# Kernel optimization log

Hardware: AMD Instinct MI355X
Metric: run time of the kernel (lower is better)

## Reference

```python
import jax, jax.numpy as jnp
import numpy as np

B, D, H = 65536, 64, 512  # batch, input_dim (even), hidden_dim; num_layers=4 -> 4 Linears


def setup_inputs() -> dict:
    key = jax.random.key(0)
    ks = jax.random.split(key, 10)
    s_in = 1.0 / np.sqrt(D)
    s_h = 1.0 / np.sqrt(H)
    return {
        "t": jnp.zeros((1,), jnp.float32),
        "x": jax.random.normal(ks[0], (B, D), jnp.float32),
        "W0": jax.random.uniform(ks[1], (D, H), jnp.float32, -s_in, s_in),
        "b0": jax.random.uniform(ks[2], (H,), jnp.float32, -s_in, s_in),
        "W1": jax.random.uniform(ks[3], (H, H), jnp.float32, -s_h, s_h),
        "b1": jax.random.uniform(ks[4], (H,), jnp.float32, -s_h, s_h),
        "W2": jax.random.uniform(ks[5], (H, H), jnp.float32, -s_h, s_h),
        "b2": jax.random.uniform(ks[6], (H,), jnp.float32, -s_h, s_h),
        "W3": jax.random.uniform(ks[7], (H, 1), jnp.float32, -s_h, s_h),
        "b3": jax.random.uniform(ks[8], (1,), jnp.float32, -s_h, s_h),
    }


def reference(t, x, W0, b0, W1, b1, W2, b2, W3, b3):
    # Hamiltonian MLP: Linear->Tanh x3, final Linear to scalar energy per sample.
    def hamiltonian_sum(xx):
        h = jnp.tanh(xx @ W0 + b0)
        h = jnp.tanh(h @ W1 + b1)
        h = jnp.tanh(h @ W2 + b2)
        return jnp.sum(h @ W3 + b3)

    gradH = jax.grad(hamiltonian_sum)(x)  # [B, D]
    n = D // 2
    # gradH @ J.T with symplectic J == concat(gradH_p, -gradH_q)
    return jnp.concatenate([gradH[:, n:], -gradH[:, :n]], axis=1)
```

## Files before the change

kernel.cpp:

```cpp
#include <hip/hip_runtime.h>
#include <hip/hip_bf16.h>

typedef unsigned short u16;
typedef short s16x8 __attribute__((ext_vector_type(8)));
typedef float f32x4 __attribute__((ext_vector_type(4)));

#define MFMA_BF16(a, b, c) __builtin_amdgcn_mfma_f32_16x16x32_bf16((a), (b), (c), 0, 0, 0)

static constexpr int D_IN   = 64;
static constexpr int H_DIM  = 512;
static constexpr int M_TILE = 64;
static constexpr int AST    = 520;
static constexpr int XST    = 72;

__device__ __forceinline__ u16 f2bf(float f) {
  unsigned u = __builtin_bit_cast(unsigned, f);
  u += 0x7fffu + ((u >> 16) & 1u);
  return (u16)(u >> 16);
}
__device__ __forceinline__ float bfb2f(unsigned bits16) {
  return __builtin_bit_cast(float, bits16 << 16);
}
__device__ __forceinline__ float fast_tanh(float x) {
  float e = __expf(2.0f * x);
  return 1.0f - 2.0f * __builtin_amdgcn_rcpf(e + 1.0f);
}

__global__ __launch_bounds__(256) void prep_weights(const float* __restrict__ W0,
                                                    const float* __restrict__ W1,
                                                    const float* __restrict__ W2,
                                                    u16* __restrict__ ws) {
  u16* p0f = ws;
  u16* p0b = p0f + D_IN * H_DIM;
  u16* p1f = p0b + D_IN * H_DIM;
  u16* p1b = p1f + H_DIM * H_DIM;
  u16* p2f = p1b + H_DIM * H_DIM;
  u16* p2b = p2f + H_DIM * H_DIM;

  __shared__ __align__(16) u16 tile[64 * 72];

  int b = blockIdx.x;
  const float* src;
  u16 *dstf, *dstb;
  int rb, cb;
  bool isW0;
  if (b < 64) {
    src = W1; dstf = p1f; dstb = p1b; rb = b >> 3; cb = b & 7; isW0 = false;
  } else if (b < 128) {
    src = W2; dstf = p2f; dstb = p2b; rb = (b - 64) >> 3; cb = (b - 64) & 7; isW0 = false;
  } else {
    src = W0; dstf = p0f; dstb = p0b; rb = 0; cb = b - 128; isW0 = true;
  }

  const int tid = threadIdx.x;

  {
    int r = tid >> 2, cc = (tid & 3) * 16;
    const float4* s4 = (const float4*)(src + (size_t)(rb * 64 + r) * 512 + cb * 64 + cc);
    unsigned pk[8];
    #pragma unroll
    for (int v = 0; v < 4; ++v) {
      float4 f = s4[v];
      pk[v * 2]     = (unsigned)f2bf(f.x) | ((unsigned)f2bf(f.y) << 16);
      pk[v * 2 + 1] = (unsigned)f2bf(f.z) | ((unsigned)f2bf(f.w) << 16);
    }
    uint4* d = (uint4*)(tile + r * 72 + cc);
    d[0] = make_uint4(pk[0], pk[1], pk[2], pk[3]);
    d[1] = make_uint4(pk[4], pk[5], pk[6], pk[7]);
  }
  __syncthreads();

  const int c   = tid >> 6;
  const int kcl = (tid >> 5) & 1;
  const int ls  = (tid * 2) & 63;
  const int q   = ls >> 4;
  const int ln  = ls & 15;

  {
    __align__(16) u16 o[16];
    #pragma unroll
    for (int half = 0; half < 2; ++half)
      #pragma unroll
      for (int j = 0; j < 8; ++j)
        o[half * 8 + j] = tile[(kcl * 32 + q * 8 + j) * 72 + c * 16 + ln + half];
    int ntg   = 4 * cb + c;
    int kc    = 2 * rb + kcl;
    int chunk = isW0 ? (ntg * 2 + kc) : (ntg * 16 + kc);
    u16* dp = dstf + ((size_t)chunk * 64 + ls) * 8;
    *(uint4*)dp       = *(const uint4*)o;
    *(uint4*)(dp + 8) = *(const uint4*)(o + 8);
  }

  {
    const u16* rp = tile + (c * 16 + ln) * 72 + kcl * 32 + q * 8;
    s16x8 r0 = *(const s16x8*)rp;
    s16x8 r1 = *(const s16x8*)(rp + 72);
    int ntg = 4 * rb + c;
    int kc  = 2 * cb + kcl;
    u16* dp = dstb + ((size_t)(ntg * 16 + kc) * 64 + ls) * 8;
    *(s16x8*)dp       = r0;
    *(s16x8*)(dp + 8) = r1;
  }
}

#define LOAD_B4(BP, KC, BR)                                                     \
  {                                                                             \
    const u16* _sr = (BP) + ((size_t)wave << 15) + ((KC) << 9) + lane * 8;      \
    _Pragma("unroll")                                                           \
    for (int s = 0; s < 4; ++s)                                                 \
      (BR)[s] = *(const s16x8*)(_sr + (s << 13));                               \
  }

#define GEMM512_REG(BP, RB)                                                     \
  {                                                                             \
    _Pragma("unroll") for (int mt = 0; mt < 4; ++mt)                            \
      _Pragma("unroll") for (int nt = 0; nt < 4; ++nt)                          \
        acc[mt][nt] = (f32x4){0.f, 0.f, 0.f, 0.f};                              \
    for (int kc2 = 0; kc2 < 8; ++kc2) {                                         \
      const int e = kc2 * 2;                                                    \
      {                                                                         \
        s16x8 a[4];                                                             \
        _Pragma("unroll")                                                       \
        for (int mt = 0; mt < 4; ++mt)                                          \
          a[mt] = *(const s16x8*)((RB) + (mt * 16 + ln) * AST + e * 32 + q * 8);\
        _Pragma("unroll")                                                       \
        for (int nt = 0; nt < 4; ++nt)                                          \
          _Pragma("unroll")                                                     \
          for (int mt = 0; mt < 4; ++mt)                                        \
            acc[mt][nt] = MFMA_BF16(a[mt], bregA[nt], acc[mt][nt]);             \
        if (kc2 < 7) LOAD_B4(BP, e + 2, bregA);                                 \
      }                                                                         \
      const int o = e + 1;                                                      \
      {                                                                         \
        s16x8 a[4];                                                             \
        _Pragma("unroll")                                                       \
        for (int mt = 0; mt < 4; ++mt)                                          \
          a[mt] = *(const s16x8*)((RB) + (mt * 16 + ln) * AST + o * 32 + q * 8);\
        _Pragma("unroll")                                                       \
        for (int nt = 0; nt < 4; ++nt)                                          \
          _Pragma("unroll")                                                     \
          for (int mt = 0; mt < 4; ++mt)                                        \
            acc[mt][nt] = MFMA_BF16(a[mt], bregB[nt], acc[mt][nt]);             \
        if (kc2 < 7) LOAD_B4(BP, o + 2, bregB);                                 \
      }                                                                         \
    }                                                                           \
  }

__global__ __launch_bounds__(512, 2) void hnn_fused(
    const float* __restrict__ x,
    const float* __restrict__ bias0,
    const float* __restrict__ bias1,
    const float* __restrict__ bias2,
    const float* __restrict__ W3,
    const u16* __restrict__ ws,
    float* __restrict__ out)
{
  const u16* p0f = ws;
  const u16* p0b = p0f + D_IN * H_DIM;
  const u16* p1f = p0b + D_IN * H_DIM;
  const u16* p1b = p1f + H_DIM * H_DIM;
  const u16* p2f = p1b + H_DIM * H_DIM;
  const u16* p2b = p2f + H_DIM * H_DIM;

  __shared__ __align__(16) u16 xs[M_TILE * XST];
  __shared__ __align__(16) u16 bufA[M_TILE * AST];
  __shared__ __align__(16) u16 bufB[M_TILE * AST];

  const int tid  = threadIdx.x;
  const int wave = tid >> 6;
  const int lane = tid & 63;
  const int ln   = lane & 15;
  const int q    = lane >> 4;
  const int nwb  = wave * 64;
  const int row0 = blockIdx.x * M_TILE;

  {
    int r = tid >> 3, c = (tid & 7) * 8;
    const float4* src = (const float4*)(x + (size_t)(row0 + r) * D_IN + c);
    float4 f0 = src[0];
    float4 f1 = src[1];
    u16* dst = xs + r * XST + c;
    dst[0] = f2bf(f0.x); dst[1] = f2bf(f0.y); dst[2] = f2bf(f0.z); dst[3] = f2bf(f0.w);
    dst[4] = f2bf(f1.x); dst[5] = f2bf(f1.y); dst[6] = f2bf(f1.z); dst[7] = f2bf(f1.w);
  }
  __syncthreads();

  f32x4 acc[4][4];
  s16x8 bregA[4], bregB[4];
  unsigned h0p[4][4][2];
  unsigned h1p[4][4][2];
  float bias[4];

  #pragma unroll
  for (int nt = 0; nt < 4; ++nt) bias[nt] = bias0[nwb + nt * 16 + ln];
  #pragma unroll
  for (int mt = 0; mt < 4; ++mt)
    #pragma unroll
    for (int nt = 0; nt < 4; ++nt) acc[mt][nt] = (f32x4){0.f, 0.f, 0.f, 0.f};
  {
    const u16* bpw0 = p0f + (wave << 12) + lane * 8;
    #pragma unroll
    for (int kc = 0; kc < 2; ++kc) {
      s16x8 a[4];
      #pragma unroll
      for (int mt = 0; mt < 4; ++mt)
        a[mt] = *(const s16x8*)(xs + (mt * 16 + ln) * XST + kc * 32 + q * 8);
      #pragma unroll
      for (int nt = 0; nt < 4; ++nt) {
        s16x8 b = *(const s16x8*)(bpw0 + (nt << 10) + (kc << 9));
        #pragma unroll
        for (int mt = 0; mt < 4; ++mt)
          acc[mt][nt] = MFMA_BF16(a[mt], b, acc[mt][nt]);
      }
    }
  }
  LOAD_B4(p1f, 0, bregA);
  LOAD_B4(p1f, 1, bregB);
  #pragma unroll
  for (int mt = 0; mt < 4; ++mt)
    #pragma unroll
    for (int nt = 0; nt < 4; ++nt) {
      int col = nwb + nt * 16 + ln;
      u16 u[4];
      #pragma unroll
      for (int r = 0; r < 4; ++r) {
        float th = fast_tanh(acc[mt][nt][r] + bias[nt]);
        u[r] = f2bf(th);
        bufA[(mt * 16 + q * 4 + r) * AST + col] = u[r];
      }
      h0p[mt][nt][0] = (unsigned)u[0] | ((unsigned)u[1] << 16);
      h0p[mt][nt][1] = (unsigned)u[2] | ((unsigned)u[3] << 16);
    }
  __syncthreads();

  #pragma unroll
  for (int nt = 0; nt < 4; ++nt) bias[nt] = bias1[nwb + nt * 16 + ln];
  GEMM512_REG(p1f, bufA);
  LOAD_B4(p2f, 0, bregA);
  LOAD_B4(p2f, 1, bregB);
  #pragma unroll
  for (int mt = 0; mt < 4; ++mt)
    #pragma unroll
    for (int nt = 0; nt < 4; ++nt) {
      int col = nwb + nt * 16 + ln;
      u16 u[4];
      #pragma unroll
      for (int r = 0; r < 4; ++r) {
        float th = fast_tanh(acc[mt][nt][r] + bias[nt]);
        u[r] = f2bf(th);
        bufB[(mt * 16 + q * 4 + r) * AST + col] = u[r];
      }
      h1p[mt][nt][0] = (unsigned)u[0] | ((unsigned)u[1] << 16);
      h1p[mt][nt][1] = (unsigned)u[2] | ((unsigned)u[3] << 16);
    }
  __syncthreads();

  #pragma unroll
  for (int nt = 0; nt < 4; ++nt) bias[nt] = bias2[nwb + nt * 16 + ln];
  float w3v[4];
  #pragma unroll
  for (int nt = 0; nt < 4; ++nt) w3v[nt] = W3[nwb + nt * 16 + ln];
  GEMM512_REG(p2f, bufB);
  LOAD_B4(p2b, 0, bregA);
  LOAD_B4(p2b, 1, bregB);
  #pragma unroll
  for (int mt = 0; mt < 4; ++mt)
    #pragma unroll
    for (int nt = 0; nt < 4; ++nt) {
      int col = nwb + nt * 16 + ln;
      #pragma unroll
      for (int r = 0; r < 4; ++r) {
        float th = fast_tanh(acc[mt][nt][r] + bias[nt]);
        float gz = w3v[nt] * (1.0f - th * th);
        bufA[(mt * 16 + q * 4 + r) * AST + col] = f2bf(gz);
      }
    }
  __syncthreads();

  GEMM512_REG(p2b, bufA);
  LOAD_B4(p1b, 0, bregA);
  LOAD_B4(p1b, 1, bregB);
  #pragma unroll
  for (int mt = 0; mt < 4; ++mt)
    #pragma unroll
    for (int nt = 0; nt < 4; ++nt) {
      int col = nwb + nt * 16 + ln;
      unsigned pa = h1p[mt][nt][0], pb = h1p[mt][nt][1];
      float hh[4] = { bfb2f(pa & 0xffffu), bfb2f(pa >> 16),
                      bfb2f(pb & 0xffffu), bfb2f(pb >> 16) };
      #pragma unroll
      for (int r = 0; r < 4; ++r) {
        float gz = acc[mt][nt][r] * (1.0f - hh[r] * hh[r]);
        bufB[(mt * 16 + q * 4 + r) * AST + col] = f2bf(gz);
      }
    }
  __syncthreads();

  GEMM512_REG(p1b, bufB);
  __syncthreads();
  #pragma unroll
  for (int mt = 0; mt < 4; ++mt)
    #pragma unroll
    for (int nt = 0; nt < 4; ++nt) {
      int col = nwb + nt * 16 + ln;
      unsigned pa = h0p[mt][nt][0], pb = h0p[mt][nt][1];
      float hh[4] = { bfb2f(pa & 0xffffu), bfb2f(pa >> 16),
                      bfb2f(pb & 0xffffu), bfb2f(pb >> 16) };
      #pragma unroll
      for (int r = 0; r < 4; ++r) {
        float gz = acc[mt][nt][r] * (1.0f - hh[r] * hh[r]);
        bufA[(mt * 16 + q * 4 + r) * AST + col] = f2bf(gz);
      }
    }
  __syncthreads();

  {
    f32x4 acc5[2];
    acc5[0] = (f32x4){0.f, 0.f, 0.f, 0.f};
    acc5[1] = (f32x4){0.f, 0.f, 0.f, 0.f};
    const int mt5 = wave & 3;
    const int nb5 = (wave >> 2) * 32;
    const u16* bp5 = p0b + ((wave >> 2) << 14) + lane * 8;
    #pragma unroll 2
    for (int kc = 0; kc < 16; ++kc) {
      s16x8 a = *(const s16x8*)(bufA + (mt5 * 16 + ln) * AST + kc * 32 + q * 8);
      #pragma unroll
      for (int nt = 0; nt < 2; ++nt) {
        s16x8 b = *(const s16x8*)(bp5 + (nt << 13) + (kc << 9));
        acc5[nt] = MFMA_BF16(a, b, acc5[nt]);
      }
    }
    #pragma unroll
    for (int nt = 0; nt < 2; ++nt) {
      int g = nb5 + nt * 16 + ln;
      int c = (g < 32) ? g + 32 : g - 32;
      float s = (g < 32) ? -1.0f : 1.0f;
      #pragma unroll
      for (int r = 0; r < 4; ++r) {
        int grow = row0 + mt5 * 16 + q * 4 + r;
        out[(size_t)grow * 64 + c] = s * acc5[nt][r];
      }
    }
  }
}

extern "C" void kernel_launch(void* const* d_in, const int* in_sizes, int n_in,
                              void* d_out, int out_size, void* d_ws, size_t ws_size,
                              hipStream_t stream) {
  const float* x  = (const float*)d_in[1];
  const float* W0 = (const float*)d_in[2];
  const float* b0 = (const float*)d_in[3];
  const float* W1 = (const float*)d_in[4];
  const float* b1 = (const float*)d_in[5];
  const float* W2 = (const float*)d_in[6];
  const float* b2 = (const float*)d_in[7];
  const float* W3 = (const float*)d_in[8];
  u16* ws = (u16*)d_ws;
  float* out = (float*)d_out;

  prep_weights<<<136, 256, 0, stream>>>(W0, W1, W2, ws);
  hnn_fused<<<65536 / M_TILE, 512, 0, stream>>>(x, b0, b1, b2, W3, ws, out);
}
```

Measured before the change: 223.9 us.

## Shrink row tile to 32 with 4 waves each covering 128 columns

Halves the block row tile to 32 and the block to 4 waves, with each wave now owning 128 hidden columns (8 N-subtiles) over 2 M-subtiles. This roughly halves LDS per block and changes the register tiling so each weight fragment loaded from global memory feeds fewer MFMAs (2 instead of 4), while doubling the number of blocks. A redundant barrier before the last backward epilogue is also removed. Register pressure rises (acc, breg and h arrays double per wave), which may limit occupancy, and per-row weight traffic from L2 doubles.

```diff
diff --git a/kernel.cpp b/kernel.cpp
--- a/kernel.cpp
+++ b/kernel.cpp
@@ -9,7 +9,7 @@
 
 static constexpr int D_IN   = 64;
 static constexpr int H_DIM  = 512;
-static constexpr int M_TILE = 64;
+static constexpr int M_TILE = 32;
 static constexpr int AST    = 520;
 static constexpr int XST    = 72;
 
@@ -103,50 +103,50 @@
   }
 }
 
-#define LOAD_B4(BP, KC, BR)                                                     \
+#define LOAD_B8(BP, KC, BR)                                                     \
   {                                                                             \
-    const u16* _sr = (BP) + ((size_t)wave << 15) + ((KC) << 9) + lane * 8;      \
+    const u16* _sr = (BP) + ((size_t)wave << 16) + ((KC) << 9) + lane * 8;      \
     _Pragma("unroll")                                                           \
-    for (int s = 0; s < 4; ++s)                                                 \
+    for (int s = 0; s < 8; ++s)                                                 \
       (BR)[s] = *(const s16x8*)(_sr + (s << 13));                               \
   }
 
 #define GEMM512_REG(BP, RB)                                                     \
   {                                                                             \
-    _Pragma("unroll") for (int mt = 0; mt < 4; ++mt)                            \
-      _Pragma("unroll") for (int nt = 0; nt < 4; ++nt)                          \
+    _Pragma("unroll") for (int mt = 0; mt < 2; ++mt)                            \
+      _Pragma("unroll") for (int nt = 0; nt < 8; ++nt)                          \
         acc[mt][nt] = (f32x4){0.f, 0.f, 0.f, 0.f};                              \
     for (int kc2 = 0; kc2 < 8; ++kc2) {                                         \
       const int e = kc2 * 2;                                                    \
       {                                                                         \
-        s16x8 a[4];                                                             \
+        s16x8 a[2];                                                             \
         _Pragma("unroll")                                                       \
-        for (int mt = 0; mt < 4; ++mt)                                          \
+        for (int mt = 0; mt < 2; ++mt)                                          \
           a[mt] = *(const s16x8*)((RB) + (mt * 16 + ln) * AST + e * 32 + q * 8);\
         _Pragma("unroll")                                                       \
-        for (int nt = 0; nt < 4; ++nt)                                          \
+        for (int nt = 0; nt < 8; ++nt)                                          \
           _Pragma("unroll")                                                     \
-          for (int mt = 0; mt < 4; ++mt)                                        \
+          for (int mt = 0; mt < 2; ++mt)                                        \
             acc[mt][nt] = MFMA_BF16(a[mt], bregA[nt], acc[mt][nt]);             \
-        if (kc2 < 7) LOAD_B4(BP, e + 2, bregA);                                 \
+        if (kc2 < 7) LOAD_B8(BP, e + 2, bregA);                                 \
       }                                                                         \
       const int o = e + 1;                                                      \
       {                                                                         \
-        s16x8 a[4];                                                             \
+        s16x8 a[2];                                                             \
         _Pragma("unroll")                                                       \
-        for (int mt = 0; mt < 4; ++mt)                                          \
+        for (int mt = 0; mt < 2; ++mt)                                          \
           a[mt] = *(const s16x8*)((RB) + (mt * 16 + ln) * AST + o * 32 + q * 8);\
         _Pragma("unroll")                                                       \
-        for (int nt = 0; nt < 4; ++nt)                                          \
+        for (int nt = 0; nt < 8; ++nt)                                          \
           _Pragma("unroll")                                                     \
-          for (int mt = 0; mt < 4; ++mt)                                        \
+          for (int mt = 0; mt < 2; ++mt)                                        \
             acc[mt][nt] = MFMA_BF16(a[mt], bregB[nt], acc[mt][nt]);             \
-        if (kc2 < 7) LOAD_B4(BP, o + 2, bregB);                                 \
+        if (kc2 < 7) LOAD_B8(BP, o + 2, bregB);                                 \
       }                                                                         \
     }                                                                           \
   }
 
-__global__ __launch_bounds__(512, 2) void hnn_fused(
+__global__ __launch_bounds__(256, 2) void hnn_fused(
     const float* __restrict__ x,
     const float* __restrict__ bias0,
     const float* __restrict__ bias1,
@@ -171,7 +171,7 @@
   const int lane = tid & 63;
   const int ln   = lane & 15;
   const int q    = lane >> 4;
-  const int nwb  = wave * 64;
+  const int nwb  = wave * 128;
   const int row0 = blockIdx.x * M_TILE;
 
   {
@@ -185,41 +185,41 @@
   }
   __syncthreads();
 
-  f32x4 acc[4][4];
-  s16x8 bregA[4], bregB[4];
-  unsigned h0p[4][4][2];
-  unsigned h1p[4][4][2];
-  float bias[4];
-
-  #pragma unroll
-  for (int nt = 0; nt < 4; ++nt) bias[nt] = bias0[nwb + nt * 16 + ln];
-  #pragma unroll
-  for (int mt = 0; mt < 4; ++mt)
-    #pragma unroll
-    for (int nt = 0; nt < 4; ++nt) acc[mt][nt] = (f32x4){0.f, 0.f, 0.f, 0.f};
-  {
-    const u16* bpw0 = p0f + (wave << 12) + lane * 8;
+  f32x4 acc[2][8];
+  s16x8 bregA[8], bregB[8];
+  unsigned h0p[2][8][2];
+  unsigned h1p[2][8][2];
+  float bias[8];
+
+  #pragma unroll
+  for (int nt = 0; nt < 8; ++nt) bias[nt] = bias0[nwb + nt * 16 + ln];
+  #pragma unroll
+  for (int mt = 0; mt < 2; ++mt)
+    #pragma unroll
+    for (int nt = 0; nt < 8; ++nt) acc[mt][nt] = (f32x4){0.f, 0.f, 0.f, 0.f};
+  {
+    const u16* bpw0 = p0f + ((size_t)wave << 13) + lane * 8;
     #pragma unroll
     for (int kc = 0; kc < 2; ++kc) {
-      s16x8 a[4];
-      #pragma unroll
-      for (int mt = 0; mt < 4; ++mt)
+      s16x8 a[2];
+      #pragma unroll
+      for (int mt = 0; mt < 2; ++mt)
         a[mt] = *(const s16x8*)(xs + (mt * 16 + ln) * XST + kc * 32 + q * 8);
       #pragma unroll
-      for (int nt = 0; nt < 4; ++nt) {
+      for (int nt = 0; nt < 8; ++nt) {
         s16x8 b = *(const s16x8*)(bpw0 + (nt << 10) + (kc << 9));
         #pragma unroll
-        for (int mt = 0; mt < 4; ++mt)
+        for (int mt = 0; mt < 2; ++mt)
           acc[mt][nt] = MFMA_BF16(a[mt], b, acc[mt][nt]);
       }
     }
   }
-  LOAD_B4(p1f, 0, bregA);
-  LOAD_B4(p1f, 1, bregB);
-  #pragma unroll
-  for (int mt = 0; mt < 4; ++mt)
-    #pragma unroll
-    for (int nt = 0; nt < 4; ++nt) {
+  LOAD_B8(p1f, 0, bregA);
+  LOAD_B8(p1f, 1, bregB);
+  #pragma unroll
+  for (int mt = 0; mt < 2; ++mt)
+    #pragma unroll
+    for (int nt = 0; nt < 8; ++nt) {
       int col = nwb + nt * 16 + ln;
       u16 u[4];
       #pragma unroll
@@ -234,14 +234,14 @@
   __syncthreads();
 
   #pragma unroll
-  for (int nt = 0; nt < 4; ++nt) bias[nt] = bias1[nwb + nt * 16 + ln];
+  for (int nt = 0; nt < 8; ++nt) bias[nt] = bias1[nwb + nt * 16 + ln];
   GEMM512_REG(p1f, bufA);
-  LOAD_B4(p2f, 0, bregA);
-  LOAD_B4(p2f, 1, bregB);
-  #pragma unroll
-  for (int mt = 0; mt < 4; ++mt)
-    #pragma unroll
-    for (int nt = 0; nt < 4; ++nt) {
+  LOAD_B8(p2f, 0, bregA);
+  LOAD_B8(p2f, 1, bregB);
+  #pragma unroll
+  for (int mt = 0; mt < 2; ++mt)
+    #pragma unroll
+    for (int nt = 0; nt < 8; ++nt) {
       int col = nwb + nt * 16 + ln;
       u16 u[4];
       #pragma unroll
@@ -256,17 +256,17 @@
   __syncthreads();
 
   #pragma unroll
-  for (int nt = 0; nt < 4; ++nt) bias[nt] = bias2[nwb + nt * 16 + ln];
-  float w3v[4];
-  #pragma unroll
-  for (int nt = 0; nt < 4; ++nt) w3v[nt] = W3[nwb + nt * 16 + ln];
+  for (int nt = 0; nt < 8; ++nt) bias[nt] = bias2[nwb + nt * 16 + ln];
+  float w3v[8];
+  #pragma unroll
+  for (int nt = 0; nt < 8; ++nt) w3v[nt] = W3[nwb + nt * 16 + ln];
   GEMM512_REG(p2f, bufB);
-  LOAD_B4(p2b, 0, bregA);
-  LOAD_B4(p2b, 1, bregB);
-  #pragma unroll
-  for (int mt = 0; mt < 4; ++mt)
-    #pragma unroll
-    for (int nt = 0; nt < 4; ++nt) {
+  LOAD_B8(p2b, 0, bregA);
+  LOAD_B8(p2b, 1, bregB);
+  #pragma unroll
+  for (int mt = 0; mt < 2; ++mt)
+    #pragma unroll
+    for (int nt = 0; nt < 8; ++nt) {
       int col = nwb + nt * 16 + ln;
       #pragma unroll
       for (int r = 0; r < 4; ++r) {
@@ -278,12 +278,12 @@
   __syncthreads();
 
   GEMM512_REG(p2b, bufA);
-  LOAD_B4(p1b, 0, bregA);
-  LOAD_B4(p1b, 1, bregB);
-  #pragma unroll
-  for (int mt = 0; mt < 4; ++mt)
-    #pragma unroll
-    for (int nt = 0; nt < 4; ++nt) {
+  LOAD_B8(p1b, 0, bregA);
+  LOAD_B8(p1b, 1, bregB);
+  #pragma unroll
+  for (int mt = 0; mt < 2; ++mt)
+    #pragma unroll
+    for (int nt = 0; nt < 8; ++nt) {
       int col = nwb + nt * 16 + ln;
       unsigned pa = h1p[mt][nt][0], pb = h1p[mt][nt][1];
       float hh[4] = { bfb2f(pa & 0xffffu), bfb2f(pa >> 16),
@@ -297,11 +297,10 @@
   __syncthreads();
 
   GEMM512_REG(p1b, bufB);
-  __syncthreads();
-  #pragma unroll
-  for (int mt = 0; mt < 4; ++mt)
-    #pragma unroll
-    for (int nt = 0; nt < 4; ++nt) {
+  #pragma unroll
+  for (int mt = 0; mt < 2; ++mt)
+    #pragma unroll
+    for (int nt = 0; nt < 8; ++nt) {
       int col = nwb + nt * 16 + ln;
       unsigned pa = h0p[mt][nt][0], pb = h0p[mt][nt][1];
       float hh[4] = { bfb2f(pa & 0xffffu), bfb2f(pa >> 16),
@@ -318,27 +317,27 @@
     f32x4 acc5[2];
     acc5[0] = (f32x4){0.f, 0.f, 0.f, 0.f};
     acc5[1] = (f32x4){0.f, 0.f, 0.f, 0.f};
-    const int mt5 = wave & 3;
-    const int nb5 = (wave >> 2) * 32;
-    const u16* bp5 = p0b + ((wave >> 2) << 14) + lane * 8;
+    const int mt5 = wave & 1;
+    const int np5 = (wave >> 1) * 2;
+    const u16* bp5 = p0b + ((size_t)np5 << 13) + lane * 8;
     #pragma unroll 2
     for (int kc = 0; kc < 16; ++kc) {
       s16x8 a = *(const s16x8*)(bufA + (mt5 * 16 + ln) * AST + kc * 32 + q * 8);
       #pragma unroll
-      for (int nt = 0; nt < 2; ++nt) {
-        s16x8 b = *(const s16x8*)(bp5 + (nt << 13) + (kc << 9));
-        acc5[nt] = MFMA_BF16(a, b, acc5[nt]);
-      }
-    }
-    #pragma unroll
-    for (int nt = 0; nt < 2; ++nt) {
-      int g = nb5 + nt * 16 + ln;
+      for (int i = 0; i < 2; ++i) {
+        s16x8 b = *(const s16x8*)(bp5 + (i << 13) + (kc << 9));
+        acc5[i] = MFMA_BF16(a, b, acc5[i]);
+      }
+    }
+    #pragma unroll
+    for (int i = 0; i < 2; ++i) {
+      int g = (np5 + i) * 16 + ln;
       int c = (g < 32) ? g + 32 : g - 32;
       float s = (g < 32) ? -1.0f : 1.0f;
       #pragma unroll
       for (int r = 0; r < 4; ++r) {
         int grow = row0 + mt5 * 16 + q * 4 + r;
-        out[(size_t)grow * 64 + c] = s * acc5[nt][r];
+        out[(size_t)grow * 64 + c] = s * acc5[i][r];
       }
     }
   }
@@ -359,5 +358,5 @@
   float* out = (float*)d_out;
 
   prep_weights<<<136, 256, 0, stream>>>(W0, W1, W2, ws);
-  hnn_fused<<<65536 / M_TILE, 512, 0, stream>>>(x, b0, b1, b2, W3, ws, out);
-}
+  hnn_fused<<<65536 / M_TILE, 256, 0, stream>>>(x, b0, b1, b2, W3, ws, out);
+}
```

Result: slower. 575.1 us (+156.9%).

## Halve row tile to 32 and raise occupancy to four blocks per CU

Applied to the files above, without the earlier changes.

Cuts the per-block row tile from 64 to 32, which halves the accumulator and saved-activation register arrays and lets launch bounds request four blocks per CU. The x load, the final input-gradient GEMM's wave-to-tile mapping and the epilogue are rewritten for the smaller tile, and one redundant barrier is dropped. The aim is more waves in flight to hide the latency of weight loads from global memory. In exchange each B-fragment loaded from global now feeds only half as many MFMAs, doubling weight traffic per row. Shared memory per block is also still fixed by AST and may limit how many blocks actually co-reside.

```diff
diff --git a/kernel.cpp b/kernel.cpp
--- a/kernel.cpp
+++ b/kernel.cpp
@@ -9,7 +9,7 @@
 
 static constexpr int D_IN   = 64;
 static constexpr int H_DIM  = 512;
-static constexpr int M_TILE = 64;
+static constexpr int M_TILE = 32;
 static constexpr int AST    = 520;
 static constexpr int XST    = 72;
 
@@ -113,40 +113,40 @@
 
 #define GEMM512_REG(BP, RB)                                                     \
   {                                                                             \
-    _Pragma("unroll") for (int mt = 0; mt < 4; ++mt)                            \
+    _Pragma("unroll") for (int mt = 0; mt < 2; ++mt)                            \
       _Pragma("unroll") for (int nt = 0; nt < 4; ++nt)                          \
         acc[mt][nt] = (f32x4){0.f, 0.f, 0.f, 0.f};                              \
     for (int kc2 = 0; kc2 < 8; ++kc2) {                                         \
       const int e = kc2 * 2;                                                    \
       {                                                                         \
-        s16x8 a[4];                                                             \
+        s16x8 a[2];                                                             \
         _Pragma("unroll")                                                       \
-        for (int mt = 0; mt < 4; ++mt)                                          \
+        for (int mt = 0; mt < 2; ++mt)                                          \
           a[mt] = *(const s16x8*)((RB) + (mt * 16 + ln) * AST + e * 32 + q * 8);\
         _Pragma("unroll")                                                       \
         for (int nt = 0; nt < 4; ++nt)                                          \
           _Pragma("unroll")                                                     \
-          for (int mt = 0; mt < 4; ++mt)                                        \
+          for (int mt = 0; mt < 2; ++mt)                                        \
             acc[mt][nt] = MFMA_BF16(a[mt], bregA[nt], acc[mt][nt]);             \
         if (kc2 < 7) LOAD_B4(BP, e + 2, bregA);                                 \
       }                                                                         \
       const int o = e + 1;                                                      \
       {                                                                         \
-        s16x8 a[4];                                                             \
+        s16x8 a[2];                                                             \
         _Pragma("unroll")                                                       \
-        for (int mt = 0; mt < 4; ++mt)                                          \
+        for (int mt = 0; mt < 2; ++mt)                                          \
           a[mt] = *(const s16x8*)((RB) + (mt * 16 + ln) * AST + o * 32 + q * 8);\
         _Pragma("unroll")                                                       \
         for (int nt = 0; nt < 4; ++nt)                                          \
           _Pragma("unroll")                                                     \
-          for (int mt = 0; mt < 4; ++mt)                                        \
+          for (int mt = 0; mt < 2; ++mt)                                        \
             acc[mt][nt] = MFMA_BF16(a[mt], bregB[nt], acc[mt][nt]);             \
         if (kc2 < 7) LOAD_B4(BP, o + 2, bregB);                                 \
       }                                                                         \
     }                                                                           \
   }
 
-__global__ __launch_bounds__(512, 2) void hnn_fused(
+__global__ __launch_bounds__(512, 4) void hnn_fused(
     const float* __restrict__ x,
     const float* __restrict__ bias0,
     const float* __restrict__ bias1,
@@ -175,41 +175,38 @@
   const int row0 = blockIdx.x * M_TILE;
 
   {
-    int r = tid >> 3, c = (tid & 7) * 8;
-    const float4* src = (const float4*)(x + (size_t)(row0 + r) * D_IN + c);
-    float4 f0 = src[0];
-    float4 f1 = src[1];
+    int r = tid >> 4, c = (tid & 15) * 4;
+    const float4 f0 = *(const float4*)(x + (size_t)(row0 + r) * D_IN + c);
     u16* dst = xs + r * XST + c;
     dst[0] = f2bf(f0.x); dst[1] = f2bf(f0.y); dst[2] = f2bf(f0.z); dst[3] = f2bf(f0.w);
-    dst[4] = f2bf(f1.x); dst[5] = f2bf(f1.y); dst[6] = f2bf(f1.z); dst[7] = f2bf(f1.w);
-  }
-  __syncthreads();
-
-  f32x4 acc[4][4];
+  }
+  __syncthreads();
+
+  f32x4 acc[2][4];
   s16x8 bregA[4], bregB[4];
-  unsigned h0p[4][4][2];
-  unsigned h1p[4][4][2];
+  unsigned h0p[2][4][2];
+  unsigned h1p[2][4][2];
   float bias[4];
 
   #pragma unroll
   for (int nt = 0; nt < 4; ++nt) bias[nt] = bias0[nwb + nt * 16 + ln];
   #pragma unroll
-  for (int mt = 0; mt < 4; ++mt)
+  for (int mt = 0; mt < 2; ++mt)
     #pragma unroll
     for (int nt = 0; nt < 4; ++nt) acc[mt][nt] = (f32x4){0.f, 0.f, 0.f, 0.f};
   {
     const u16* bpw0 = p0f + (wave << 12) + lane * 8;
     #pragma unroll
     for (int kc = 0; kc < 2; ++kc) {
-      s16x8 a[4];
-      #pragma unroll
-      for (int mt = 0; mt < 4; ++mt)
+      s16x8 a[2];
+      #pragma unroll
+      for (int mt = 0; mt < 2; ++mt)
         a[mt] = *(const s16x8*)(xs + (mt * 16 + ln) * XST + kc * 32 + q * 8);
       #pragma unroll
       for (int nt = 0; nt < 4; ++nt) {
         s16x8 b = *(const s16x8*)(bpw0 + (nt << 10) + (kc << 9));
         #pragma unroll
-        for (int mt = 0; mt < 4; ++mt)
+        for (int mt = 0; mt < 2; ++mt)
           acc[mt][nt] = MFMA_BF16(a[mt], b, acc[mt][nt]);
       }
     }
@@ -217,7 +214,7 @@
   LOAD_B4(p1f, 0, bregA);
   LOAD_B4(p1f, 1, bregB);
   #pragma unroll
-  for (int mt = 0; mt < 4; ++mt)
+  for (int mt = 0; mt < 2; ++mt)
     #pragma unroll
     for (int nt = 0; nt < 4; ++nt) {
       int col = nwb + nt * 16 + ln;
@@ -239,7 +236,7 @@
   LOAD_B4(p2f, 0, bregA);
   LOAD_B4(p2f, 1, bregB);
   #pragma unroll
-  for (int mt = 0; mt < 4; ++mt)
+  for (int mt = 0; mt < 2; ++mt)
     #pragma unroll
     for (int nt = 0; nt < 4; ++nt) {
       int col = nwb + nt * 16 + ln;
@@ -264,7 +261,7 @@
   LOAD_B4(p2b, 0, bregA);
   LOAD_B4(p2b, 1, bregB);
   #pragma unroll
-  for (int mt = 0; mt < 4; ++mt)
+  for (int mt = 0; mt < 2; ++mt)
     #pragma unroll
     for (int nt = 0; nt < 4; ++nt) {
       int col = nwb + nt * 16 + ln;
@@ -281,7 +278,7 @@
   LOAD_B4(p1b, 0, bregA);
   LOAD_B4(p1b, 1, bregB);
   #pragma unroll
-  for (int mt = 0; mt < 4; ++mt)
+  for (int mt = 0; mt < 2; ++mt)
     #pragma unroll
     for (int nt = 0; nt < 4; ++nt) {
       int col = nwb + nt * 16 + ln;
@@ -297,9 +294,8 @@
   __syncthreads();
 
   GEMM512_REG(p1b, bufB);
-  __syncthreads();
-  #pragma unroll
-  for (int mt = 0; mt < 4; ++mt)
+  #pragma unroll
+  for (int mt = 0; mt < 2; ++mt)
     #pragma unroll
     for (int nt = 0; nt < 4; ++nt) {
       int col = nwb + nt * 16 + ln;
@@ -315,31 +311,23 @@
   __syncthreads();
 
   {
-    f32x4 acc5[2];
-    acc5[0] = (f32x4){0.f, 0.f, 0.f, 0.f};
-    acc5[1] = (f32x4){0.f, 0.f, 0.f, 0.f};
-    const int mt5 = wave & 3;
-    const int nb5 = (wave >> 2) * 32;
-    const u16* bp5 = p0b + ((wave >> 2) << 14) + lane * 8;
+    f32x4 acc5 = (f32x4){0.f, 0.f, 0.f, 0.f};
+    const int mt5 = wave & 1;
+    const int c5  = wave >> 1;
+    const u16* bp5 = p0b + ((size_t)c5 << 13) + lane * 8;
     #pragma unroll 2
     for (int kc = 0; kc < 16; ++kc) {
       s16x8 a = *(const s16x8*)(bufA + (mt5 * 16 + ln) * AST + kc * 32 + q * 8);
-      #pragma unroll
-      for (int nt = 0; nt < 2; ++nt) {
-        s16x8 b = *(const s16x8*)(bp5 + (nt << 13) + (kc << 9));
-        acc5[nt] = MFMA_BF16(a, b, acc5[nt]);
-      }
-    }
-    #pragma unroll
-    for (int nt = 0; nt < 2; ++nt) {
-      int g = nb5 + nt * 16 + ln;
-      int c = (g < 32) ? g + 32 : g - 32;
-      float s = (g < 32) ? -1.0f : 1.0f;
-      #pragma unroll
-      for (int r = 0; r < 4; ++r) {
-        int grow = row0 + mt5 * 16 + q * 4 + r;
-        out[(size_t)grow * 64 + c] = s * acc5[nt][r];
-      }
+      s16x8 b = *(const s16x8*)(bp5 + (kc << 9));
+      acc5 = MFMA_BF16(a, b, acc5);
+    }
+    int g = c5 * 16 + ln;
+    int cc = (g < 32) ? g + 32 : g - 32;
+    float sg = (g < 32) ? -1.0f : 1.0f;
+    #pragma unroll
+    for (int r = 0; r < 4; ++r) {
+      int grow = row0 + mt5 * 16 + q * 4 + r;
+      out[(size_t)grow * 64 + cc] = sg * acc5[r];
     }
   }
 }
```

After: 364.0 us. 62.6% more time.
